# Kernel optimization log

Hardware: AMD Instinct MI355X
Metric: run time of the kernel (lower is better)

Reference implementation:

```python
import jax, jax.numpy as jnp
import numpy as np

TOTAL_DIM = 64  # 16+16+16+8+8
HIDDEN = 4 * TOTAL_DIM
NUM_HEADS = 8


def _fourier(x, num_freqs):
    # Dyadic Fourier features: sin/cos of 2^j * x for j in [0, num_freqs).
    # Output dim = input_dim * num_freqs * 2 (matches embed_dim in the module).
    freqs = 2.0 ** jnp.arange(num_freqs, dtype=x.dtype)  # (F,)
    phase = x[..., :, None] * freqs                       # (..., in, F)
    out = jnp.concatenate([jnp.sin(phase), jnp.cos(phase)], axis=-1)  # (..., in, 2F)
    return out.reshape(x.shape[:-1] + (-1,))


def setup_inputs() -> dict:
    key = jax.random.key(0)
    k1, k2, k3, k4, k5, k6 = jax.random.split(key, 6)
    B, Nq, Nk, D = 8, 256, 256, 10
    query_states = jax.random.normal(k1, (B, Nq, D), dtype=jnp.float32)
    key_states = jax.random.normal(k2, (B, Nk, D), dtype=jnp.float32)
    W1 = jax.random.normal(k3, (TOTAL_DIM, HIDDEN), dtype=jnp.float32) / np.sqrt(TOTAL_DIM)
    b1 = jnp.zeros((HIDDEN,), dtype=jnp.float32)
    W2 = jax.random.normal(k4, (HIDDEN, NUM_HEADS), dtype=jnp.float32) / np.sqrt(HIDDEN)
    b2 = jnp.zeros((NUM_HEADS,), dtype=jnp.float32)
    return {"query_states": query_states, "key_states": key_states,
            "W1": W1, "b1": b1, "W2": W2, "b2": b2}


def _features(query_states, key_states):
    # Slice per-ship fields, then broadcast pairwise: q -> (B,Nq,1,*), k -> (B,1,Nk,*)
    q_team = query_states[:, :, None, 0]          # (B,Nq,1)
    k_team = key_states[:, None, :, 0]            # (B,1,Nk)
    q_pos = query_states[:, :, None, 3:5]
    k_pos = key_states[:, None, :, 3:5]
    q_vel = query_states[:, :, None, 5:7]
    k_vel = key_states[:, None, :, 5:7]
    q_att = query_states[:, :, None, 7:9]
    k_att = key_states[:, None, :, 7:9]

    delta_pos = k_pos - q_pos                     # (B,Nq,Nk,2)
    delta_vel = k_vel - q_vel                     # (B,Nq,Nk,2)
    feat_delta_input = jnp.concatenate([delta_pos, delta_vel], axis=-1)  # (B,Nq,Nk,4)

    dist_sq = jnp.sum(delta_pos ** 2, axis=-1, keepdims=True)
    dist = jnp.sqrt(dist_sq + 1e-6)
    inv_dist = 1.0 / (dist + 0.1)
    feat_dist_input = jnp.concatenate([dist, inv_dist], axis=-1)         # (B,Nq,Nk,2)

    bearing = delta_pos / (dist + 1e-6)
    ata = jnp.sum(bearing * q_att, axis=-1, keepdims=True)
    aspect = jnp.sum(bearing * k_att, axis=-1, keepdims=True)
    feat_angle_input = jnp.concatenate([ata, aspect], axis=-1)           # (B,Nq,Nk,2)

    dot_dp_dv = jnp.sum(delta_pos * delta_vel, axis=-1, keepdims=True)
    speed_sq = jnp.sum(delta_vel ** 2, axis=-1, keepdims=True)
    ttca = jnp.tanh(jax.nn.relu(-dot_dp_dv / (speed_sq + 1e-6)))
    feat_intercept_input = jnp.concatenate([ttca, dist], axis=-1)        # (B,Nq,Nk,2)

    same_team = (q_team == k_team).astype(query_states.dtype)[..., None]
    q_speed = jnp.linalg.norm(q_vel, axis=-1, keepdims=True)
    k_speed = jnp.linalg.norm(k_vel, axis=-1, keepdims=True)
    delta_speed = k_speed - q_speed
    feat_team_input = jnp.concatenate([same_team, delta_speed], axis=-1)  # (B,Nq,Nk,2)

    out_dist = _fourier(feat_dist_input, 4)        # 16
    out_angle = _fourier(feat_angle_input, 4)      # 16
    out_delta = _fourier(feat_delta_input, 2)      # 16
    out_intercept = _fourier(feat_intercept_input, 2)  # 8
    out_team = _fourier(feat_team_input, 2)        # 8
    return jnp.concatenate([out_dist, out_angle, out_delta, out_intercept, out_team], axis=-1)


def reference(query_states, key_states, W1, b1, W2, b2):
    combined = _features(query_states, key_states)          # (B,Nq,Nk,64)
    h = jax.nn.silu(combined @ W1 + b1)                     # (B,Nq,Nk,256)
    bias = h @ W2 + b2                                      # (B,Nq,Nk,H)
    return jnp.transpose(bias, (0, 3, 1, 2))                # (B,H,Nq,Nk)
```

## Files before the change

kernel.cpp:

```cpp
#include <hip/hip_runtime.h>
#include <math.h>

#define NB 8
#define NQ 256
#define NK 256
#define DIN 10
#define FDIM 64
#define HIDDEN 256
#define NH 8
#define ROWS_PER_BLK 4

#define FSTRIDE 64
#define HSTRIDE 264
#define W2S 264

typedef float f32x4 __attribute__((ext_vector_type(4)));
typedef short bf16x8 __attribute__((ext_vector_type(8)));

__device__ __forceinline__ short f2bf(float f) {
    return (short)((__float_as_uint(f) + 0x8000u) >> 16);
}
__device__ __forceinline__ unsigned pack2(float a, float b) {
    unsigned ua = __float_as_uint(a) + 0x8000u;
    unsigned ub = __float_as_uint(b) + 0x8000u;
    return __builtin_amdgcn_perm(ub, ua, 0x07060302);
}

__device__ __forceinline__ void four4(float x, float* dst) {
    float s1 = __sinf(x), c1 = __cosf(x);
    float s2 = 2.f * s1 * c1, c2 = 1.f - 2.f * s1 * s1;
    float s4 = 2.f * s2 * c2, c4 = 1.f - 2.f * s2 * s2;
    float s8 = 2.f * s4 * c4, c8 = 1.f - 2.f * s4 * s4;
    dst[0] = s1; dst[1] = s2; dst[2] = s4; dst[3] = s8;
    dst[4] = c1; dst[5] = c2; dst[6] = c4; dst[7] = c8;
}
__device__ __forceinline__ void four2(float x, float* dst) {
    float s1 = __sinf(x), c1 = __cosf(x);
    dst[0] = s1; dst[1] = 2.f * s1 * c1;
    dst[2] = c1; dst[3] = 1.f - 2.f * s1 * s1;
}

__global__ __launch_bounds__(256, 2) void relfeat_mfma_kernel(
    const float* __restrict__ q, const float* __restrict__ k,
    const float* __restrict__ W1, const float* __restrict__ b1,
    const float* __restrict__ W2, const float* __restrict__ b2,
    float* __restrict__ out)
{
    __shared__ __align__(16) short feat_s[NK * FSTRIDE];
    __shared__ __align__(16) short h_s[64 * HSTRIDE];
    __shared__ __align__(16) short w2_s[8 * W2S];

    const int t = threadIdx.x;
    const int wave = t >> 6;
    const int lane15 = t & 15;
    const int quad = (t >> 4) & 3;
    const int b = blockIdx.x >> 6;
    const int i0 = (blockIdx.x & 63) * ROWS_PER_BLK;

    const float* kp = k + ((size_t)b * NK + t) * DIN;
    const float k0 = kp[0], k3 = kp[3], k4 = kp[4], k5 = kp[5], k6 = kp[6],
                k7 = kp[7], k8 = kp[8];

#pragma unroll
    for (int o = 0; o < NH; ++o)
        w2_s[o * W2S + t] = f2bf(-0.69314718f * W2[t * NH + o]);

    const int n0 = wave * 64;
    bf16x8 w1f[4][2];
#pragma unroll
    for (int nt = 0; nt < 4; ++nt)
#pragma unroll
        for (int ks = 0; ks < 2; ++ks) {
            const float* wp = W1 + (size_t)(ks * 32 + quad * 8) * HIDDEN
                              + (n0 + nt * 16 + lane15);
            bf16x8 v;
#pragma unroll
            for (int e = 0; e < 8; ++e)
                v[e] = f2bf(-1.44269504f * wp[(size_t)e * HIDDEN]);
            w1f[nt][ks] = v;
        }
    float4 b1q[4];
#pragma unroll
    for (int nt = 0; nt < 4; ++nt) {
        float4 bb = *(const float4*)&b1[n0 + nt * 16 + quad * 4];
        b1q[nt] = make_float4(-1.44269504f * bb.x, -1.44269504f * bb.y,
                              -1.44269504f * bb.z, -1.44269504f * bb.w);
    }
    const float b2v = (lane15 < NH) ? b2[lane15] : 0.f;

    const int sw = t & 7;
    const int swr = lane15 & 7;

#pragma unroll 1
    for (int row = 0; row < ROWS_PER_BLK; ++row) {
        const int i = i0 + row;

        {
            const float* qp = q + ((size_t)b * NQ + i) * DIN;
            const float q0 = qp[0], q3 = qp[3], q4 = qp[4], q5 = qp[5],
                        q6 = qp[6], q7 = qp[7], q8 = qp[8];

            const float dpx = k3 - q3, dpy = k4 - q4;
            const float dvx = k5 - q5, dvy = k6 - q6;
            const float dist = sqrtf(dpx * dpx + dpy * dpy + 1e-6f);
            const float inv_dist = 1.0f / (dist + 0.1f);
            const float inv_d2 = 1.0f / (dist + 1e-6f);
            const float bear_x = dpx * inv_d2, bear_y = dpy * inv_d2;
            const float ata = bear_x * q7 + bear_y * q8;
            const float aspect = bear_x * k7 + bear_y * k8;
            const float dot_dp_dv = dpx * dvx + dpy * dvy;
            const float speed_sq = dvx * dvx + dvy * dvy;
            const float ttca = tanhf(fmaxf(0.f, -dot_dp_dv / (speed_sq + 1e-6f)));
            const float same_team = (q0 == k0) ? 1.f : 0.f;
            const float q_speed = sqrtf(q5 * q5 + q6 * q6);
            const float k_speed = sqrtf(k5 * k5 + k6 * k6);
            const float delta_speed = k_speed - q_speed;

            float feat[FDIM];
            four4(dist,        feat + 0);
            four4(inv_dist,    feat + 8);
            four4(ata,         feat + 16);
            four4(aspect,      feat + 24);
            four2(dpx,         feat + 32);
            four2(dpy,         feat + 36);
            four2(dvx,         feat + 40);
            four2(dvy,         feat + 44);
            four2(ttca,        feat + 48);
            four2(dist,        feat + 52);
            four2(same_team,   feat + 56);
            four2(delta_speed, feat + 60);

#pragma unroll
            for (int c8 = 0; c8 < 8; ++c8) {
                uint4 v;
                v.x = pack2(feat[c8 * 8 + 0], feat[c8 * 8 + 1]);
                v.y = pack2(feat[c8 * 8 + 2], feat[c8 * 8 + 3]);
                v.z = pack2(feat[c8 * 8 + 4], feat[c8 * 8 + 5]);
                v.w = pack2(feat[c8 * 8 + 6], feat[c8 * 8 + 7]);
                *(uint4*)&feat_s[t * FSTRIDE + ((c8 ^ sw) * 8)] = v;
            }
        }
        __syncthreads();

#pragma unroll 1
        for (int c = 0; c < 4; ++c) {
            const int p0 = c * 64;

            f32x4 acc[4][4];
#pragma unroll
            for (int nt = 0; nt < 4; ++nt)
#pragma unroll
                for (int mt = 0; mt < 4; ++mt)
                    acc[nt][mt] = (f32x4){b1q[nt].x, b1q[nt].y, b1q[nt].z, b1q[nt].w};
#pragma unroll
            for (int ks = 0; ks < 2; ++ks)
#pragma unroll
                for (int mt = 0; mt < 4; ++mt) {
                    const int r2 = p0 + mt * 16 + lane15;
                    const bf16x8 fb = *(const bf16x8*)
                        &feat_s[r2 * FSTRIDE + (((ks * 4 + quad) ^ swr) * 8)];
#pragma unroll
                    for (int nt = 0; nt < 4; ++nt)
                        acc[nt][mt] = __builtin_amdgcn_mfma_f32_16x16x32_bf16(
                            w1f[nt][ks], fb, acc[nt][mt], 0, 0, 0);
                }

            __syncthreads();

#pragma unroll
            for (int nt = 0; nt < 4; ++nt)
#pragma unroll
                for (int mt = 0; mt < 4; ++mt) {
                    const int pair = mt * 16 + lane15;
                    const int hbase = n0 + nt * 16 + quad * 4;
                    float s[4];
#pragma unroll
                    for (int r = 0; r < 4; ++r) {
                        const float a = acc[nt][mt][r];
                        const float e = __builtin_amdgcn_exp2f(a);
                        s[r] = a * __builtin_amdgcn_rcpf(1.f + e);
                    }
                    uint2 pk;
                    pk.x = pack2(s[0], s[1]);
                    pk.y = pack2(s[2], s[3]);
                    *(uint2*)&h_s[pair * HSTRIDE + hbase] = pk;
                }
            __syncthreads();

            {
                const int pw = wave * 16;
                f32x4 acc2 = (f32x4){b2v, b2v, b2v, b2v};
#pragma unroll
                for (int ks = 0; ks < 8; ++ks) {
                    const bf16x8 ha = *(const bf16x8*)&h_s[(pw + lane15) * HSTRIDE
                                                            + ks * 32 + quad * 8];
                    const bf16x8 wb = *(const bf16x8*)&w2_s[(lane15 & 7) * W2S
                                                             + ks * 32 + quad * 8];
                    acc2 = __builtin_amdgcn_mfma_f32_16x16x32_bf16(ha, wb, acc2, 0, 0, 0);
                }
                if (lane15 < NH) {
                    float* op = out + (((size_t)b * NH + lane15) * NQ + i) * NK
                                + (p0 + pw + quad * 4);
                    *(float4*)op = make_float4(acc2[0], acc2[1], acc2[2], acc2[3]);
                }
            }
        }
    }
}

extern "C" void kernel_launch(void* const* d_in, const int* in_sizes, int n_in,
                              void* d_out, int out_size, void* d_ws, size_t ws_size,
                              hipStream_t stream) {
    const float* q  = (const float*)d_in[0];
    const float* k  = (const float*)d_in[1];
    const float* W1 = (const float*)d_in[2];
    const float* b1 = (const float*)d_in[3];
    const float* W2 = (const float*)d_in[4];
    const float* b2 = (const float*)d_in[5];
    float* out = (float*)d_out;

    dim3 grid(NB * NQ / ROWS_PER_BLK);
    dim3 block(NK);
    relfeat_mfma_kernel<<<grid, block, 0, stream>>>(q, k, W1, b1, W2, b2, out);
}
```

Measured before the change: 113.3 us.

## Give each wave its own key rows and prepack W1 to bf16

Work is repartitioned so each wave owns 64 key positions and computes all 256 hidden units for them. Feature, hidden-activation and output data therefore stay wave-private, which removes the block-wide barriers inside the row and chunk loops. W1 is pre-converted once per call into a swizzled bf16 layout in workspace by a small prep kernel, and the main kernel loads A fragments from global memory or cache on every MFMA instead of holding them in registers. The b1 bias moves to shared memory. In exchange, each chunk now issues many more global loads for W1, relies on cache hits, and adds an extra kernel launch.

```diff
diff --git a/kernel.cpp b/kernel.cpp
--- a/kernel.cpp
+++ b/kernel.cpp
@@ -10,9 +10,7 @@
 #define NH 8
 #define ROWS_PER_BLK 4
 
-#define FSTRIDE 64
-#define HSTRIDE 264
-#define W2S 264
+#define HS2 264
 
 typedef float f32x4 __attribute__((ext_vector_type(4)));
 typedef short bf16x8 __attribute__((ext_vector_type(8)));
@@ -40,22 +38,40 @@
     dst[2] = c1; dst[3] = 1.f - 2.f * s1 * s1;
 }
 
+__global__ __launch_bounds__(256, 1) void prep_w1(
+    const float* __restrict__ W1, short* __restrict__ w1t)
+{
+    const int t = threadIdx.x;
+    const int fb = blockIdx.x;
+    float v[8];
+#pragma unroll
+    for (int e = 0; e < 8; ++e)
+        v[e] = -1.44269504f * W1[(size_t)(fb * 8 + e) * HIDDEN + t];
+    uint4 pk;
+    pk.x = pack2(v[0], v[1]); pk.y = pack2(v[2], v[3]);
+    pk.z = pack2(v[4], v[5]); pk.w = pack2(v[6], v[7]);
+    *(uint4*)&w1t[t * FDIM + ((fb ^ (t & 7)) * 8)] = pk;
+}
+
 __global__ __launch_bounds__(256, 2) void relfeat_mfma_kernel(
     const float* __restrict__ q, const float* __restrict__ k,
-    const float* __restrict__ W1, const float* __restrict__ b1,
+    const short* __restrict__ w1t, const float* __restrict__ b1,
     const float* __restrict__ W2, const float* __restrict__ b2,
     float* __restrict__ out)
 {
-    __shared__ __align__(16) short feat_s[NK * FSTRIDE];
-    __shared__ __align__(16) short h_s[64 * HSTRIDE];
-    __shared__ __align__(16) short w2_s[8 * W2S];
+    __shared__ __align__(16) short feat_s[NK * FDIM];
+    __shared__ __align__(16) short h_s[4 * 16 * HS2];
+    __shared__ __align__(16) short w2_s[8 * HS2];
+    __shared__ __align__(16) float b1_s[HIDDEN];
 
     const int t = threadIdx.x;
     const int wave = t >> 6;
-    const int lane15 = t & 15;
+    const int l15 = t & 15;
     const int quad = (t >> 4) & 3;
     const int b = blockIdx.x >> 6;
     const int i0 = (blockIdx.x & 63) * ROWS_PER_BLK;
+    const int swr = l15 & 7;
+    const int hbase = wave * 16 * HS2;
 
     const float* kp = k + ((size_t)b * NK + t) * DIN;
     const float k0 = kp[0], k3 = kp[3], k4 = kp[4], k5 = kp[5], k6 = kp[6],
@@ -63,33 +79,11 @@
 
 #pragma unroll
     for (int o = 0; o < NH; ++o)
-        w2_s[o * W2S + t] = f2bf(-0.69314718f * W2[t * NH + o]);
-
-    const int n0 = wave * 64;
-    bf16x8 w1f[4][2];
-#pragma unroll
-    for (int nt = 0; nt < 4; ++nt)
-#pragma unroll
-        for (int ks = 0; ks < 2; ++ks) {
-            const float* wp = W1 + (size_t)(ks * 32 + quad * 8) * HIDDEN
-                              + (n0 + nt * 16 + lane15);
-            bf16x8 v;
-#pragma unroll
-            for (int e = 0; e < 8; ++e)
-                v[e] = f2bf(-1.44269504f * wp[(size_t)e * HIDDEN]);
-            w1f[nt][ks] = v;
-        }
-    float4 b1q[4];
-#pragma unroll
-    for (int nt = 0; nt < 4; ++nt) {
-        float4 bb = *(const float4*)&b1[n0 + nt * 16 + quad * 4];
-        b1q[nt] = make_float4(-1.44269504f * bb.x, -1.44269504f * bb.y,
-                              -1.44269504f * bb.z, -1.44269504f * bb.w);
-    }
-    const float b2v = (lane15 < NH) ? b2[lane15] : 0.f;
-
-    const int sw = t & 7;
-    const int swr = lane15 & 7;
+        w2_s[o * HS2 + t] = f2bf(-0.69314718f * W2[t * NH + o]);
+    b1_s[t] = -1.44269504f * b1[t];
+    const float b2v = (l15 < NH) ? b2[l15] : 0.f;
+
+    __syncthreads();
 
 #pragma unroll 1
     for (int row = 0; row < ROWS_PER_BLK; ++row) {
@@ -130,6 +124,7 @@
             four2(same_team,   feat + 56);
             four2(delta_speed, feat + 60);
 
+            const int sw = t & 7;
 #pragma unroll
             for (int c8 = 0; c8 < 8; ++c8) {
                 uint4 v;
@@ -137,72 +132,65 @@
                 v.y = pack2(feat[c8 * 8 + 2], feat[c8 * 8 + 3]);
                 v.z = pack2(feat[c8 * 8 + 4], feat[c8 * 8 + 5]);
                 v.w = pack2(feat[c8 * 8 + 6], feat[c8 * 8 + 7]);
-                *(uint4*)&feat_s[t * FSTRIDE + ((c8 ^ sw) * 8)] = v;
+                *(uint4*)&feat_s[t * FDIM + ((c8 ^ sw) * 8)] = v;
             }
         }
-        __syncthreads();
 
 #pragma unroll 1
         for (int c = 0; c < 4; ++c) {
-            const int p0 = c * 64;
-
-            f32x4 acc[4][4];
-#pragma unroll
-            for (int nt = 0; nt < 4; ++nt)
-#pragma unroll
-                for (int mt = 0; mt < 4; ++mt)
-                    acc[nt][mt] = (f32x4){b1q[nt].x, b1q[nt].y, b1q[nt].z, b1q[nt].w};
-#pragma unroll
-            for (int ks = 0; ks < 2; ++ks)
-#pragma unroll
-                for (int mt = 0; mt < 4; ++mt) {
-                    const int r2 = p0 + mt * 16 + lane15;
-                    const bf16x8 fb = *(const bf16x8*)
-                        &feat_s[r2 * FSTRIDE + (((ks * 4 + quad) ^ swr) * 8)];
-#pragma unroll
-                    for (int nt = 0; nt < 4; ++nt)
-                        acc[nt][mt] = __builtin_amdgcn_mfma_f32_16x16x32_bf16(
-                            w1f[nt][ks], fb, acc[nt][mt], 0, 0, 0);
-                }
-
-            __syncthreads();
-
-#pragma unroll
-            for (int nt = 0; nt < 4; ++nt)
-#pragma unroll
-                for (int mt = 0; mt < 4; ++mt) {
-                    const int pair = mt * 16 + lane15;
-                    const int hbase = n0 + nt * 16 + quad * 4;
-                    float s[4];
-#pragma unroll
-                    for (int r = 0; r < 4; ++r) {
-                        const float a = acc[nt][mt][r];
-                        const float e = __builtin_amdgcn_exp2f(a);
-                        s[r] = a * __builtin_amdgcn_rcpf(1.f + e);
-                    }
-                    uint2 pk;
-                    pk.x = pack2(s[0], s[1]);
-                    pk.y = pack2(s[2], s[3]);
-                    *(uint2*)&h_s[pair * HSTRIDE + hbase] = pk;
-                }
-            __syncthreads();
-
-            {
-                const int pw = wave * 16;
-                f32x4 acc2 = (f32x4){b2v, b2v, b2v, b2v};
-#pragma unroll
-                for (int ks = 0; ks < 8; ++ks) {
-                    const bf16x8 ha = *(const bf16x8*)&h_s[(pw + lane15) * HSTRIDE
-                                                            + ks * 32 + quad * 8];
-                    const bf16x8 wb = *(const bf16x8*)&w2_s[(lane15 & 7) * W2S
-                                                             + ks * 32 + quad * 8];
-                    acc2 = __builtin_amdgcn_mfma_f32_16x16x32_bf16(ha, wb, acc2, 0, 0, 0);
-                }
-                if (lane15 < NH) {
-                    float* op = out + (((size_t)b * NH + lane15) * NQ + i) * NK
-                                + (p0 + pw + quad * 4);
-                    *(float4*)op = make_float4(acc2[0], acc2[1], acc2[2], acc2[3]);
-                }
+            const int p0 = wave * 64 + c * 16;
+
+            f32x4 acc[16];
+#pragma unroll
+            for (int mt = 0; mt < 16; ++mt) acc[mt] = (f32x4){0.f, 0.f, 0.f, 0.f};
+
+            const bf16x8 fb0 = *(const bf16x8*)
+                &feat_s[(p0 + l15) * FDIM + ((quad ^ swr) * 8)];
+            const bf16x8 fb1 = *(const bf16x8*)
+                &feat_s[(p0 + l15) * FDIM + (((4 + quad) ^ swr) * 8)];
+#pragma unroll
+            for (int mt = 0; mt < 16; ++mt) {
+                const bf16x8 a0 = *(const bf16x8*)
+                    &w1t[(mt * 16 + l15) * FDIM + ((quad ^ swr) * 8)];
+                acc[mt] = __builtin_amdgcn_mfma_f32_16x16x32_bf16(a0, fb0, acc[mt], 0, 0, 0);
+            }
+#pragma unroll
+            for (int mt = 0; mt < 16; ++mt) {
+                const bf16x8 a1 = *(const bf16x8*)
+                    &w1t[(mt * 16 + l15) * FDIM + (((4 + quad) ^ swr) * 8)];
+                acc[mt] = __builtin_amdgcn_mfma_f32_16x16x32_bf16(a1, fb1, acc[mt], 0, 0, 0);
+            }
+
+#pragma unroll
+            for (int mt = 0; mt < 16; ++mt) {
+                const float4 bv = *(const float4*)&b1_s[mt * 16 + quad * 4];
+                const float a0 = acc[mt][0] + bv.x;
+                const float a1 = acc[mt][1] + bv.y;
+                const float a2 = acc[mt][2] + bv.z;
+                const float a3 = acc[mt][3] + bv.w;
+                const float s0 = a0 * __builtin_amdgcn_rcpf(1.f + __builtin_amdgcn_exp2f(a0));
+                const float s1 = a1 * __builtin_amdgcn_rcpf(1.f + __builtin_amdgcn_exp2f(a1));
+                const float s2 = a2 * __builtin_amdgcn_rcpf(1.f + __builtin_amdgcn_exp2f(a2));
+                const float s3 = a3 * __builtin_amdgcn_rcpf(1.f + __builtin_amdgcn_exp2f(a3));
+                uint2 pk;
+                pk.x = pack2(s0, s1);
+                pk.y = pack2(s2, s3);
+                *(uint2*)&h_s[hbase + l15 * HS2 + mt * 16 + quad * 4] = pk;
+            }
+
+            f32x4 acc2 = (f32x4){b2v, b2v, b2v, b2v};
+#pragma unroll
+            for (int k2 = 0; k2 < 8; ++k2) {
+                const bf16x8 ha = *(const bf16x8*)
+                    &h_s[hbase + l15 * HS2 + k2 * 32 + quad * 8];
+                const bf16x8 wb = *(const bf16x8*)
+                    &w2_s[(l15 & 7) * HS2 + k2 * 32 + quad * 8];
+                acc2 = __builtin_amdgcn_mfma_f32_16x16x32_bf16(ha, wb, acc2, 0, 0, 0);
+            }
+            if (l15 < NH) {
+                float* op = out + (((size_t)b * NH + l15) * NQ + i) * NK
+                            + p0 + quad * 4;
+                *(float4*)op = make_float4(acc2[0], acc2[1], acc2[2], acc2[3]);
             }
         }
     }
@@ -218,8 +206,10 @@
     const float* W2 = (const float*)d_in[4];
     const float* b2 = (const float*)d_in[5];
     float* out = (float*)d_out;
-
+    short* w1t = (short*)d_ws;
+
+    prep_w1<<<dim3(8), dim3(256), 0, stream>>>(W1, w1t);
     dim3 grid(NB * NQ / ROWS_PER_BLK);
     dim3 block(NK);
-    relfeat_mfma_kernel<<<grid, block, 0, stream>>>(q, k, W1, b1, W2, b2, out);
-}
+    relfeat_mfma_kernel<<<grid, block, 0, stream>>>(q, k, w1t, b1, W2, b2, out);
+}
```

New measurement: 204.1 us. 1.8x slower.

## Double-buffer hidden tile, halve chunk size, keep W2 fragments in registers

Applied to the files above, without the earlier changes.

The pair loop now runs over 32-pair chunks with a double-buffered hidden tile in shared memory. This removes one of the two block barriers per chunk. Only two waves run the second MFMA for each chunk, alternating by parity, so their work can overlap with the next chunk's first GEMM. W2 fragments are held in registers instead of being read from shared memory. In exchange, each chunk has less MFMA work per barrier, two waves sit idle during each second GEMM, and register pressure rises, which could hurt occupancy at launch bounds of 2.

```diff
diff --git a/kernel.cpp b/kernel.cpp
--- a/kernel.cpp
+++ b/kernel.cpp
@@ -12,7 +12,6 @@
 
 #define FSTRIDE 64
 #define HSTRIDE 264
-#define W2S 264
 
 typedef float f32x4 __attribute__((ext_vector_type(4)));
 typedef short bf16x8 __attribute__((ext_vector_type(8)));
@@ -47,23 +46,31 @@
     float* __restrict__ out)
 {
     __shared__ __align__(16) short feat_s[NK * FSTRIDE];
-    __shared__ __align__(16) short h_s[64 * HSTRIDE];
-    __shared__ __align__(16) short w2_s[8 * W2S];
+    __shared__ __align__(16) short h_s[2 * 32 * HSTRIDE];
 
     const int t = threadIdx.x;
     const int wave = t >> 6;
-    const int lane15 = t & 15;
+    const int l15 = t & 15;
     const int quad = (t >> 4) & 3;
     const int b = blockIdx.x >> 6;
     const int i0 = (blockIdx.x & 63) * ROWS_PER_BLK;
+    const int swr = l15 & 7;
 
     const float* kp = k + ((size_t)b * NK + t) * DIN;
     const float k0 = kp[0], k3 = kp[3], k4 = kp[4], k5 = kp[5], k6 = kp[6],
                 k7 = kp[7], k8 = kp[8];
 
-#pragma unroll
-    for (int o = 0; o < NH; ++o)
-        w2_s[o * W2S + t] = f2bf(-0.69314718f * W2[t * NH + o]);
+    bf16x8 w2f[8];
+#pragma unroll
+    for (int k2 = 0; k2 < 8; ++k2) {
+        bf16x8 v;
+#pragma unroll
+        for (int e = 0; e < 8; ++e)
+            v[e] = f2bf(-0.69314718f *
+                        W2[(size_t)(k2 * 32 + quad * 8 + e) * NH + (l15 & 7)]);
+        w2f[k2] = v;
+    }
+    const float b2v = (l15 < NH) ? b2[l15] : 0.f;
 
     const int n0 = wave * 64;
     bf16x8 w1f[4][2];
@@ -72,7 +79,7 @@
 #pragma unroll
         for (int ks = 0; ks < 2; ++ks) {
             const float* wp = W1 + (size_t)(ks * 32 + quad * 8) * HIDDEN
-                              + (n0 + nt * 16 + lane15);
+                              + (n0 + nt * 16 + l15);
             bf16x8 v;
 #pragma unroll
             for (int e = 0; e < 8; ++e)
@@ -86,10 +93,6 @@
         b1q[nt] = make_float4(-1.44269504f * bb.x, -1.44269504f * bb.y,
                               -1.44269504f * bb.z, -1.44269504f * bb.w);
     }
-    const float b2v = (lane15 < NH) ? b2[lane15] : 0.f;
-
-    const int sw = t & 7;
-    const int swr = lane15 & 7;
 
 #pragma unroll 1
     for (int row = 0; row < ROWS_PER_BLK; ++row) {
@@ -130,6 +133,7 @@
             four2(same_team,   feat + 56);
             four2(delta_speed, feat + 60);
 
+            const int sw = t & 7;
 #pragma unroll
             for (int c8 = 0; c8 < 8; ++c8) {
                 uint4 v;
@@ -143,20 +147,21 @@
         __syncthreads();
 
 #pragma unroll 1
-        for (int c = 0; c < 4; ++c) {
-            const int p0 = c * 64;
-
-            f32x4 acc[4][4];
+        for (int hc = 0; hc < 8; ++hc) {
+            const int p0 = hc * 32;
+            short* hb = &h_s[(hc & 1) * 32 * HSTRIDE];
+
+            f32x4 acc[4][2];
 #pragma unroll
             for (int nt = 0; nt < 4; ++nt)
 #pragma unroll
-                for (int mt = 0; mt < 4; ++mt)
+                for (int mt = 0; mt < 2; ++mt)
                     acc[nt][mt] = (f32x4){b1q[nt].x, b1q[nt].y, b1q[nt].z, b1q[nt].w};
 #pragma unroll
             for (int ks = 0; ks < 2; ++ks)
 #pragma unroll
-                for (int mt = 0; mt < 4; ++mt) {
-                    const int r2 = p0 + mt * 16 + lane15;
+                for (int mt = 0; mt < 2; ++mt) {
+                    const int r2 = p0 + mt * 16 + l15;
                     const bf16x8 fb = *(const bf16x8*)
                         &feat_s[r2 * FSTRIDE + (((ks * 4 + quad) ^ swr) * 8)];
 #pragma unroll
@@ -165,13 +170,11 @@
                             w1f[nt][ks], fb, acc[nt][mt], 0, 0, 0);
                 }
 
-            __syncthreads();
-
 #pragma unroll
             for (int nt = 0; nt < 4; ++nt)
 #pragma unroll
-                for (int mt = 0; mt < 4; ++mt) {
-                    const int pair = mt * 16 + lane15;
+                for (int mt = 0; mt < 2; ++mt) {
+                    const int pair = mt * 16 + l15;
                     const int hbase = n0 + nt * 16 + quad * 4;
                     float s[4];
 #pragma unroll
@@ -183,23 +186,22 @@
                     uint2 pk;
                     pk.x = pack2(s[0], s[1]);
                     pk.y = pack2(s[2], s[3]);
-                    *(uint2*)&h_s[pair * HSTRIDE + hbase] = pk;
+                    *(uint2*)&hb[pair * HSTRIDE + hbase] = pk;
                 }
             __syncthreads();
 
-            {
-                const int pw = wave * 16;
+            if ((wave >> 1) == (hc & 1)) {
+                const int pw = (wave & 1) * 16;
                 f32x4 acc2 = (f32x4){b2v, b2v, b2v, b2v};
 #pragma unroll
-                for (int ks = 0; ks < 8; ++ks) {
-                    const bf16x8 ha = *(const bf16x8*)&h_s[(pw + lane15) * HSTRIDE
-                                                            + ks * 32 + quad * 8];
-                    const bf16x8 wb = *(const bf16x8*)&w2_s[(lane15 & 7) * W2S
-                                                             + ks * 32 + quad * 8];
-                    acc2 = __builtin_amdgcn_mfma_f32_16x16x32_bf16(ha, wb, acc2, 0, 0, 0);
-                }
-                if (lane15 < NH) {
-                    float* op = out + (((size_t)b * NH + lane15) * NQ + i) * NK
+                for (int k2 = 0; k2 < 8; ++k2) {
+                    const bf16x8 ha = *(const bf16x8*)
+                        &hb[(pw + l15) * HSTRIDE + k2 * 32 + quad * 8];
+                    acc2 = __builtin_amdgcn_mfma_f32_16x16x32_bf16(
+                        ha, w2f[k2], acc2, 0, 0, 0);
+                }
+                if (l15 < NH) {
+                    float* op = out + (((size_t)b * NH + l15) * NQ + i) * NK
                                 + (p0 + pw + quad * 4);
                     *(float4*)op = make_float4(acc2[0], acc2[1], acc2[2], acc2[3]);
                 }
```

Measured after the change: 115.4 us. No clear change (+1.9%).
